# Performance work log

Measured on AMD Instinct MI355X. Metric: run time of the kernel, lower is better.

Reference implementation:

```python
import jax, jax.numpy as jnp
import numpy as np

N_NODES = 50000
LN_EPS = 1e-5


def gcn_conv(x, src, dst, norm, W, b):
    # PyG GCNConv: h = x @ W, then symmetric-normalized scatter-add, then bias.
    h = x @ W                                   # [N, out]
    msg = h[src] * norm[:, None]                # [E+N, out] gathered, scaled
    out = jax.ops.segment_sum(msg, dst, num_segments=N_NODES)
    return out + b


def layer_norm(x, gamma, beta):
    mu = jnp.mean(x, axis=-1, keepdims=True)
    var = jnp.var(x, axis=-1, keepdims=True)
    return (x - mu) * jax.lax.rsqrt(var + LN_EPS) * gamma + beta


def setup_inputs() -> dict:
    key = jax.random.key(0)
    ks = jax.random.split(key, 8)
    N, E, D = N_NODES, 1600000, 128
    x = jax.random.normal(ks[0], (N, D), dtype=jnp.float32)
    edge_index = jax.random.randint(ks[1], (2, E), 0, N, dtype=jnp.int64)
    s = 1.0 / np.sqrt(D)
    return {
        "x": x,
        "edge_index": edge_index,
        "W1": jax.random.uniform(ks[2], (D, D), jnp.float32, -s, s),
        "b1": jnp.zeros((D,), jnp.float32),
        "g1": jnp.ones((D,), jnp.float32),
        "be1": jnp.zeros((D,), jnp.float32),
        "W2": jax.random.uniform(ks[3], (D, D), jnp.float32, -s, s),
        "b2": jnp.zeros((D,), jnp.float32),
        "g2": jnp.ones((D,), jnp.float32),
        "be2": jnp.zeros((D,), jnp.float32),
    }


def reference(x, edge_index, W1, b1, g1, be1, W2, b2, g2, be2):
    # Add self-loops (PyG GCNConv default add_self_loops=True)
    sl = jnp.arange(N_NODES, dtype=edge_index.dtype)
    src = jnp.concatenate([edge_index[0], sl])
    dst = jnp.concatenate([edge_index[1], sl])
    # Symmetric normalization: deg^{-1/2}[src] * deg^{-1/2}[dst]
    deg = jax.ops.segment_sum(jnp.ones_like(src, dtype=x.dtype), dst,
                              num_segments=N_NODES)
    dinv = jnp.where(deg > 0, jax.lax.rsqrt(deg), 0.0)
    norm = dinv[src] * dinv[dst]

    h = gcn_conv(x, src, dst, norm, W1, b1)
    h = jax.nn.elu(layer_norm(h, g1, be1))
    h = gcn_conv(h, src, dst, norm, W2, b2)
    h = jax.nn.elu(layer_norm(h, g2, be2))
    return h
```

## Files before the change

kernel.cpp:

```cpp
#include <hip/hip_runtime.h>
#include <hip/hip_bf16.h>
#include <math.h>

#define N_NODES 50000
#define D 128
#define LN_EPS 1e-5f
#define NB 391
#define CHUNK 4096

typedef unsigned int u32;
typedef unsigned short u16;
typedef __attribute__((ext_vector_type(8))) short bf16x8;
typedef __attribute__((ext_vector_type(4))) float f32x4;

static __device__ __forceinline__ u16 f2bf(float f) {
    union { float f; unsigned u; } v; v.f = f;
    unsigned r = v.u + 0x7fff + ((v.u >> 16) & 1);
    return (u16)(r >> 16);
}
static __device__ __forceinline__ float bf2f(u16 b) {
    union { unsigned u; float f; } v; v.u = ((unsigned)b) << 16;
    return v.f;
}

__global__ __launch_bounds__(256) void bucket_hist(const int* __restrict__ dstA,
                                                   u32* __restrict__ bucketCount, int E) {
    __shared__ u32 hist[NB];
    for (int b = threadIdx.x; b < NB; b += 256) hist[b] = 0;
    __syncthreads();
    int stride = gridDim.x * 256;
    for (int e = blockIdx.x * 256 + threadIdx.x; e < E; e += stride)
        atomicAdd(&hist[((u32)dstA[e]) >> 7], 1u);
    __syncthreads();
    for (int b = threadIdx.x; b < NB; b += 256)
        if (hist[b]) atomicAdd(&bucketCount[b], hist[b]);
}

__global__ void scan_kernel(const u32* __restrict__ bucketCount, u32* __restrict__ ebStart,
                            u32* __restrict__ ebCursor, u32* __restrict__ csrStart) {
    __shared__ u32 s[512];
    int t = threadIdx.x;
    u32 my = (t < NB) ? bucketCount[t] : 0u;
    s[t] = my;
    __syncthreads();
    for (int off = 1; off < 512; off <<= 1) {
        u32 v = s[t] + ((t >= off) ? s[t - off] : 0u);
        __syncthreads();
        s[t] = v;
        __syncthreads();
    }
    if (t < NB) {
        u32 excl = s[t] - my;
        ebStart[t]  = excl;
        ebCursor[t] = excl;
        csrStart[t] = excl + 128u * (u32)t;
    }
}

__global__ __launch_bounds__(256) void partition_kernel(const int* __restrict__ srcA,
                                                        const int* __restrict__ dstA,
                                                        u32* __restrict__ ebCursor,
                                                        u32* __restrict__ ebuf, int E) {
    __shared__ u32 cntA[NB], cntB[NB], base[NB];
    int t = threadIdx.x;
    for (int b = t; b < NB; b += 256) { cntA[b] = 0; cntB[b] = 0; }
    __syncthreads();
    int e0 = blockIdx.x * CHUNK;
    int e1 = min(e0 + CHUNK, E);
    for (int e = e0 + t; e < e1; e += 256)
        atomicAdd(&cntA[((u32)dstA[e]) >> 7], 1u);
    __syncthreads();
    for (int b = t; b < NB; b += 256)
        if (cntA[b]) base[b] = atomicAdd(&ebCursor[b], cntA[b]);
    __syncthreads();
    for (int e = e0 + t; e < e1; e += 256) {
        u32 d = (u32)dstA[e], sv = (u32)srcA[e];
        u32 b = d >> 7;
        u32 off = atomicAdd(&cntB[b], 1u);
        ebuf[base[b] + off] = (sv << 16) | d;
    }
}

__global__ __launch_bounds__(256) void bucket_build(const u32* __restrict__ ebuf,
                                                    const u32* __restrict__ ebStart,
                                                    const u32* __restrict__ ebEnd,
                                                    const u32* __restrict__ csrStart,
                                                    u16* __restrict__ csr_src,
                                                    int* __restrict__ startArr,
                                                    int* __restrict__ deg,
                                                    float* __restrict__ dinv) {
    int b = blockIdx.x, t = threadIdx.x;
    int nodeBase = b << 7;
    int nNodes = min(128, N_NODES - nodeBase);
    __shared__ u32 cnt[128], sc[128], cur[128];
    if (t < 128) cnt[t] = 0;
    __syncthreads();
    u32 eb0 = ebStart[b], eb1 = ebEnd[b];
    for (u32 e = eb0 + t; e < eb1; e += 256)
        atomicAdd(&cnt[ebuf[e] & 127u], 1u);
    __syncthreads();
    if (t < 128) sc[t] = (t < nNodes) ? cnt[t] + 1u : 0u;
    __syncthreads();
    for (int off = 1; off < 128; off <<= 1) {
        u32 v = 0;
        if (t < 128) v = sc[t] + ((t >= off) ? sc[t - off] : 0u);
        __syncthreads();
        if (t < 128) sc[t] = v;
        __syncthreads();
    }
    u32 cs = csrStart[b];
    if (t < nNodes) {
        u32 val = cnt[t] + 1u;
        u32 excl = sc[t] - val;
        int i = nodeBase + t;
        deg[i] = (int)val;
        dinv[i] = rsqrtf((float)val);
        u32 sa = cs + excl;
        startArr[i] = (int)sa;
        csr_src[sa] = (u16)i;
        cur[t] = excl + 1u;
    }
    __syncthreads();
    for (u32 e = eb0 + t; e < eb1; e += 256) {
        u32 p = ebuf[e];
        u32 pos = atomicAdd(&cur[p & 127u], 1u);
        csr_src[cs + pos] = (u16)(p >> 16);
    }
}

static __device__ __forceinline__ bf16x8 packf8(const float* p) {
    float4 f0 = *(const float4*)p;
    float4 f1 = *(const float4*)(p + 4);
    bf16x8 r;
    r[0] = (short)f2bf(f0.x); r[1] = (short)f2bf(f0.y);
    r[2] = (short)f2bf(f0.z); r[3] = (short)f2bf(f0.w);
    r[4] = (short)f2bf(f1.x); r[5] = (short)f2bf(f1.y);
    r[6] = (short)f2bf(f1.z); r[7] = (short)f2bf(f1.w);
    return r;
}

template <int SRCF32>
__global__ __launch_bounds__(256) void gemm_mfma(const void* __restrict__ Xv,
                                                 const float* __restrict__ W,
                                                 u16* __restrict__ H, int n) {
    __shared__ __align__(16) u16 WT[D][136];
    for (int idx = threadIdx.x; idx < D * D; idx += 256) {
        int k = idx >> 7, c = idx & 127;
        WT[c][k] = f2bf(W[idx]);
    }
    __syncthreads();

    int lane = threadIdx.x & 63;
    int wid  = threadIdx.x >> 6;
    int r    = lane & 15;
    int kg   = lane >> 4;

    int rb0 = blockIdx.x * 4 + wid;
    int nrb = gridDim.x * 4;
    for (int rb = rb0; rb < n / 16; rb += nrb) {
        int row0 = rb * 16;
        bf16x8 a0, a1, a2, a3;
        if (SRCF32) {
            const float* xp = (const float*)Xv + (size_t)(row0 + r) * D + kg * 8;
            a0 = packf8(xp); a1 = packf8(xp + 32); a2 = packf8(xp + 64); a3 = packf8(xp + 96);
        } else {
            const u16* xp = (const u16*)Xv + (size_t)(row0 + r) * D + kg * 8;
            a0 = *(const bf16x8*)(xp);      a1 = *(const bf16x8*)(xp + 32);
            a2 = *(const bf16x8*)(xp + 64); a3 = *(const bf16x8*)(xp + 96);
        }
#pragma unroll
        for (int tile = 0; tile < 8; ++tile) {
            const u16* wp = &WT[tile * 16 + r][kg * 8];
            f32x4 acc = {0.f, 0.f, 0.f, 0.f};
            acc = __builtin_amdgcn_mfma_f32_16x16x32_bf16(a0, *(const bf16x8*)(wp),      acc, 0, 0, 0);
            acc = __builtin_amdgcn_mfma_f32_16x16x32_bf16(a1, *(const bf16x8*)(wp + 32), acc, 0, 0, 0);
            acc = __builtin_amdgcn_mfma_f32_16x16x32_bf16(a2, *(const bf16x8*)(wp + 64), acc, 0, 0, 0);
            acc = __builtin_amdgcn_mfma_f32_16x16x32_bf16(a3, *(const bf16x8*)(wp + 96), acc, 0, 0, 0);
#pragma unroll
            for (int i = 0; i < 4; ++i)
                H[(size_t)(row0 + kg * 4 + i) * D + tile * 16 + r] = f2bf(acc[i]);
        }
    }
}

template <int WRITE_BF16>
__global__ __launch_bounds__(256) void agg_ln_elu(
        const u16* __restrict__ H, const u16* __restrict__ csr_src,
        const int* __restrict__ startArr, const int* __restrict__ deg,
        const float* __restrict__ dinv,
        const float* __restrict__ bias, const float* __restrict__ gamma,
        const float* __restrict__ beta, void* __restrict__ outv) {
    int lane = threadIdx.x & 63;
    int wid  = threadIdx.x >> 6;
    int half = lane >> 5;
    int l    = lane & 31;
    int node = blockIdx.x * 8 + wid * 2 + half;

    int s    = startArr[node];
    int cnt  = deg[node];
    float dn = dinv[node];
    int c0   = l * 4;

    float a0 = 0.f, a1 = 0.f, a2 = 0.f, a3 = 0.f;
    int j = 0;
    for (; j + 4 <= cnt; j += 4) {
        u32 s0 = csr_src[s + j],     s1 = csr_src[s + j + 1];
        u32 s2 = csr_src[s + j + 2], s3 = csr_src[s + j + 3];
        float w0 = dinv[s0] * dn, w1 = dinv[s1] * dn;
        float w2 = dinv[s2] * dn, w3 = dinv[s3] * dn;
        ushort4 g0 = *(const ushort4*)&H[(size_t)s0 * D + c0];
        ushort4 g1 = *(const ushort4*)&H[(size_t)s1 * D + c0];
        ushort4 g2 = *(const ushort4*)&H[(size_t)s2 * D + c0];
        ushort4 g3 = *(const ushort4*)&H[(size_t)s3 * D + c0];
        a0 = fmaf(w0, bf2f(g0.x), a0); a1 = fmaf(w0, bf2f(g0.y), a1);
        a2 = fmaf(w0, bf2f(g0.z), a2); a3 = fmaf(w0, bf2f(g0.w), a3);
        a0 = fmaf(w1, bf2f(g1.x), a0); a1 = fmaf(w1, bf2f(g1.y), a1);
        a2 = fmaf(w1, bf2f(g1.z), a2); a3 = fmaf(w1, bf2f(g1.w), a3);
        a0 = fmaf(w2, bf2f(g2.x), a0); a1 = fmaf(w2, bf2f(g2.y), a1);
        a2 = fmaf(w2, bf2f(g2.z), a2); a3 = fmaf(w2, bf2f(g2.w), a3);
        a0 = fmaf(w3, bf2f(g3.x), a0); a1 = fmaf(w3, bf2f(g3.y), a1);
        a2 = fmaf(w3, bf2f(g3.z), a2); a3 = fmaf(w3, bf2f(g3.w), a3);
    }
    for (; j < cnt; ++j) {
        u32 s0 = csr_src[s + j];
        float w0 = dinv[s0] * dn;
        ushort4 g0 = *(const ushort4*)&H[(size_t)s0 * D + c0];
        a0 = fmaf(w0, bf2f(g0.x), a0); a1 = fmaf(w0, bf2f(g0.y), a1);
        a2 = fmaf(w0, bf2f(g0.z), a2); a3 = fmaf(w0, bf2f(g0.w), a3);
    }

    float4 bv = *(const float4*)&bias[c0];
    a0 += bv.x; a1 += bv.y; a2 += bv.z; a3 += bv.w;

    float sum = a0 + a1 + a2 + a3;
    float sq  = a0 * a0 + a1 * a1 + a2 * a2 + a3 * a3;
#pragma unroll
    for (int m = 16; m > 0; m >>= 1) {
        sum += __shfl_xor(sum, m, 64);
        sq  += __shfl_xor(sq,  m, 64);
    }
    float mean = sum * (1.f / 128.f);
    float var  = sq * (1.f / 128.f) - mean * mean;
    float rstd = rsqrtf(var + LN_EPS);

    float4 gv = *(const float4*)&gamma[c0];
    float4 ev = *(const float4*)&beta[c0];
    float y0 = (a0 - mean) * rstd * gv.x + ev.x;
    float y1 = (a1 - mean) * rstd * gv.y + ev.y;
    float y2 = (a2 - mean) * rstd * gv.z + ev.z;
    float y3 = (a3 - mean) * rstd * gv.w + ev.w;
    y0 = y0 > 0.f ? y0 : expm1f(y0);
    y1 = y1 > 0.f ? y1 : expm1f(y1);
    y2 = y2 > 0.f ? y2 : expm1f(y2);
    y3 = y3 > 0.f ? y3 : expm1f(y3);

    if (WRITE_BF16) {
        ushort4 o;
        o.x = f2bf(y0); o.y = f2bf(y1); o.z = f2bf(y2); o.w = f2bf(y3);
        *(ushort4*)((u16*)outv + (size_t)node * D + c0) = o;
    } else {
        float4 o; o.x = y0; o.y = y1; o.z = y2; o.w = y3;
        *(float4*)((float*)outv + (size_t)node * D + c0) = o;
    }
}

extern "C" void kernel_launch(void* const* d_in, const int* in_sizes, int n_in,
                              void* d_out, int out_size, void* d_ws, size_t ws_size,
                              hipStream_t stream) {
    const float* x   = (const float*)d_in[0];
    const int*  eidx = (const int*)d_in[1];
    const float* W1  = (const float*)d_in[2];
    const float* b1  = (const float*)d_in[3];
    const float* g1  = (const float*)d_in[4];
    const float* be1 = (const float*)d_in[5];
    const float* W2  = (const float*)d_in[6];
    const float* b2  = (const float*)d_in[7];
    const float* g2  = (const float*)d_in[8];
    const float* be2 = (const float*)d_in[9];

    int E = in_sizes[1] / 2;
    const int* srcA = eidx;
    const int* dstA = eidx + E;

    char* p = (char*)d_ws;
    auto alloc = [&](size_t bytes) {
        char* r = p;
        p += (bytes + 255) & ~(size_t)255;
        return r;
    };
    u32*   bucketCount = (u32*)alloc((size_t)NB * 4);
    u32*   ebStart     = (u32*)alloc((size_t)NB * 4);
    u32*   ebCursor    = (u32*)alloc((size_t)NB * 4);
    u32*   csrStart    = (u32*)alloc((size_t)NB * 4);
    u32*   ebuf        = (u32*)alloc((size_t)E * 4);
    u16*   csr_src     = (u16*)alloc((size_t)(E + N_NODES) * 2);
    int*   startArr    = (int*)alloc((size_t)N_NODES * 4);
    int*   deg         = (int*)alloc((size_t)N_NODES * 4);
    float* dinv        = (float*)alloc((size_t)N_NODES * 4);
    u16*   h           = (u16*)alloc((size_t)N_NODES * D * 2);
    u16*   x2b         = (u16*)alloc((size_t)N_NODES * D * 2);
    float* outp        = (float*)d_out;

    int pb = (E + CHUNK - 1) / CHUNK;
    int gb = (N_NODES / 16 + 3) / 4;
    int ab = N_NODES / 8;

    hipMemsetAsync(bucketCount, 0, (size_t)NB * 4, stream);
    bucket_hist     <<<512, 256, 0, stream>>>(dstA, bucketCount, E);
    scan_kernel     <<<1, 512, 0, stream>>>(bucketCount, ebStart, ebCursor, csrStart);
    partition_kernel<<<pb, 256, 0, stream>>>(srcA, dstA, ebCursor, ebuf, E);
    bucket_build    <<<NB, 256, 0, stream>>>(ebuf, ebStart, ebCursor, csrStart,
                                             csr_src, startArr, deg, dinv);

    gemm_mfma<1>  <<<gb, 256, 0, stream>>>(x, W1, h, N_NODES);
    agg_ln_elu<1> <<<ab, 256, 0, stream>>>(h, csr_src, startArr, deg, dinv,
                                           b1, g1, be1, x2b);
    gemm_mfma<0>  <<<gb, 256, 0, stream>>>(x2b, W2, h, N_NODES);
    agg_ln_elu<0> <<<ab, 256, 0, stream>>>(h, csr_src, startArr, deg, dinv,
                                           b2, g2, be2, outp);
}
```

Before: 295.3 us.

## Fuse GEMM1 with bucket histogram, drop scan kernel, widen aggregation unroll

The first GEMM and the destination-bucket histogram now run as one launch, with the blocks split by role. The separate scan kernel is removed: each partition block recomputes the bucket prefix scan itself, and bucket_build sums its prefix directly from the bucket counts. This cuts kernel launches and the serial single-block stage, at the cost of redundant scan work in every block. Separately, the aggregation loop is unrolled to 8 edges with two accumulator sets for more memory-level parallelism, and the final fp32 output uses nontemporal stores.

```diff
diff --git a/kernel.cpp b/kernel.cpp
--- a/kernel.cpp
+++ b/kernel.cpp
@@ -7,6 +7,8 @@
 #define LN_EPS 1e-5f
 #define NB 391
 #define CHUNK 4096
+#define GB 782
+#define HB 512
 
 typedef unsigned int u32;
 typedef unsigned short u16;
@@ -23,57 +25,130 @@
     return v.f;
 }
 
-__global__ __launch_bounds__(256) void bucket_hist(const int* __restrict__ dstA,
-                                                   u32* __restrict__ bucketCount, int E) {
+static __device__ __forceinline__ bf16x8 packf8(const float* p) {
+    float4 f0 = *(const float4*)p;
+    float4 f1 = *(const float4*)(p + 4);
+    bf16x8 r;
+    r[0] = (short)f2bf(f0.x); r[1] = (short)f2bf(f0.y);
+    r[2] = (short)f2bf(f0.z); r[3] = (short)f2bf(f0.w);
+    r[4] = (short)f2bf(f1.x); r[5] = (short)f2bf(f1.y);
+    r[6] = (short)f2bf(f1.z); r[7] = (short)f2bf(f1.w);
+    return r;
+}
+
+__global__ __launch_bounds__(256) void gemm1_hist(const float* __restrict__ X,
+                                                  const float* __restrict__ W,
+                                                  u16* __restrict__ H,
+                                                  const int* __restrict__ dstA,
+                                                  u32* __restrict__ bucketCount, int E) {
+    __shared__ __align__(16) u16 WT[D][136];
     __shared__ u32 hist[NB];
-    for (int b = threadIdx.x; b < NB; b += 256) hist[b] = 0;
-    __syncthreads();
-    int stride = gridDim.x * 256;
-    for (int e = blockIdx.x * 256 + threadIdx.x; e < E; e += stride)
-        atomicAdd(&hist[((u32)dstA[e]) >> 7], 1u);
-    __syncthreads();
-    for (int b = threadIdx.x; b < NB; b += 256)
-        if (hist[b]) atomicAdd(&bucketCount[b], hist[b]);
-}
-
-__global__ void scan_kernel(const u32* __restrict__ bucketCount, u32* __restrict__ ebStart,
-                            u32* __restrict__ ebCursor, u32* __restrict__ csrStart) {
-    __shared__ u32 s[512];
+
+    if (blockIdx.x >= GB) {
+        for (int b = threadIdx.x; b < NB; b += 256) hist[b] = 0;
+        __syncthreads();
+        int stride = HB * 256;
+        for (int e = (blockIdx.x - GB) * 256 + threadIdx.x; e < E; e += stride)
+            atomicAdd(&hist[((u32)dstA[e]) >> 7], 1u);
+        __syncthreads();
+        for (int b = threadIdx.x; b < NB; b += 256)
+            if (hist[b]) atomicAdd(&bucketCount[b], hist[b]);
+        return;
+    }
+    for (int idx = threadIdx.x; idx < D * D; idx += 256) {
+        int k = idx >> 7, c = idx & 127;
+        WT[c][k] = f2bf(W[idx]);
+    }
+    __syncthreads();
+
+    int lane = threadIdx.x & 63;
+    int wid  = threadIdx.x >> 6;
+    int r    = lane & 15;
+    int kg   = lane >> 4;
+
+    for (int rb = blockIdx.x * 4 + wid; rb < N_NODES / 16; rb += GB * 4) {
+        int row0 = rb * 16;
+        const float* xp = X + (size_t)(row0 + r) * D + kg * 8;
+        bf16x8 a0 = packf8(xp);      bf16x8 a1 = packf8(xp + 32);
+        bf16x8 a2 = packf8(xp + 64); bf16x8 a3 = packf8(xp + 96);
+#pragma unroll
+        for (int tile = 0; tile < 8; ++tile) {
+            const u16* wp = &WT[tile * 16 + r][kg * 8];
+            f32x4 acc = {0.f, 0.f, 0.f, 0.f};
+            acc = __builtin_amdgcn_mfma_f32_16x16x32_bf16(a0, *(const bf16x8*)(wp),      acc, 0, 0, 0);
+            acc = __builtin_amdgcn_mfma_f32_16x16x32_bf16(a1, *(const bf16x8*)(wp + 32), acc, 0, 0, 0);
+            acc = __builtin_amdgcn_mfma_f32_16x16x32_bf16(a2, *(const bf16x8*)(wp + 64), acc, 0, 0, 0);
+            acc = __builtin_amdgcn_mfma_f32_16x16x32_bf16(a3, *(const bf16x8*)(wp + 96), acc, 0, 0, 0);
+#pragma unroll
+            for (int i = 0; i < 4; ++i)
+                H[(size_t)(row0 + kg * 4 + i) * D + tile * 16 + r] = f2bf(acc[i]);
+        }
+    }
+}
+
+__global__ __launch_bounds__(256) void gemm_mfma(const u16* __restrict__ Xb,
+                                                 const float* __restrict__ W,
+                                                 u16* __restrict__ H) {
+    __shared__ __align__(16) u16 WT[D][136];
+    for (int idx = threadIdx.x; idx < D * D; idx += 256) {
+        int k = idx >> 7, c = idx & 127;
+        WT[c][k] = f2bf(W[idx]);
+    }
+    __syncthreads();
+    int lane = threadIdx.x & 63;
+    int wid  = threadIdx.x >> 6;
+    int r    = lane & 15;
+    int kg   = lane >> 4;
+    for (int rb = blockIdx.x * 4 + wid; rb < N_NODES / 16; rb += GB * 4) {
+        int row0 = rb * 16;
+        const u16* xp = Xb + (size_t)(row0 + r) * D + kg * 8;
+        bf16x8 a0 = *(const bf16x8*)(xp);      bf16x8 a1 = *(const bf16x8*)(xp + 32);
+        bf16x8 a2 = *(const bf16x8*)(xp + 64); bf16x8 a3 = *(const bf16x8*)(xp + 96);
+#pragma unroll
+        for (int tile = 0; tile < 8; ++tile) {
+            const u16* wp = &WT[tile * 16 + r][kg * 8];
+            f32x4 acc = {0.f, 0.f, 0.f, 0.f};
+            acc = __builtin_amdgcn_mfma_f32_16x16x32_bf16(a0, *(const bf16x8*)(wp),      acc, 0, 0, 0);
+            acc = __builtin_amdgcn_mfma_f32_16x16x32_bf16(a1, *(const bf16x8*)(wp + 32), acc, 0, 0, 0);
+            acc = __builtin_amdgcn_mfma_f32_16x16x32_bf16(a2, *(const bf16x8*)(wp + 64), acc, 0, 0, 0);
+            acc = __builtin_amdgcn_mfma_f32_16x16x32_bf16(a3, *(const bf16x8*)(wp + 96), acc, 0, 0, 0);
+#pragma unroll
+            for (int i = 0; i < 4; ++i)
+                H[(size_t)(row0 + kg * 4 + i) * D + tile * 16 + r] = f2bf(acc[i]);
+        }
+    }
+}
+
+__global__ __launch_bounds__(512) void partition_kernel(const int* __restrict__ srcA,
+                                                        const int* __restrict__ dstA,
+                                                        const u32* __restrict__ bucketCount,
+                                                        u32* __restrict__ relCursor,
+                                                        u32* __restrict__ ebuf, int E) {
+    __shared__ u32 sc[512];
+    __shared__ u32 ebS[NB], cntA[NB], cntB[NB], base[NB];
     int t = threadIdx.x;
-    u32 my = (t < NB) ? bucketCount[t] : 0u;
-    s[t] = my;
+    u32 bc = (t < NB) ? bucketCount[t] : 0u;
+    sc[t] = bc;
+    for (int b = t; b < NB; b += 512) { cntA[b] = 0; cntB[b] = 0; }
     __syncthreads();
     for (int off = 1; off < 512; off <<= 1) {
-        u32 v = s[t] + ((t >= off) ? s[t - off] : 0u);
-        __syncthreads();
-        s[t] = v;
-        __syncthreads();
-    }
-    if (t < NB) {
-        u32 excl = s[t] - my;
-        ebStart[t]  = excl;
-        ebCursor[t] = excl;
-        csrStart[t] = excl + 128u * (u32)t;
-    }
-}
-
-__global__ __launch_bounds__(256) void partition_kernel(const int* __restrict__ srcA,
-                                                        const int* __restrict__ dstA,
-                                                        u32* __restrict__ ebCursor,
-                                                        u32* __restrict__ ebuf, int E) {
-    __shared__ u32 cntA[NB], cntB[NB], base[NB];
-    int t = threadIdx.x;
-    for (int b = t; b < NB; b += 256) { cntA[b] = 0; cntB[b] = 0; }
-    __syncthreads();
+        u32 v = sc[t] + ((t >= off) ? sc[t - off] : 0u);
+        __syncthreads();
+        sc[t] = v;
+        __syncthreads();
+    }
+    if (t < NB) ebS[t] = sc[t] - bc;
+    __syncthreads();
+
     int e0 = blockIdx.x * CHUNK;
     int e1 = min(e0 + CHUNK, E);
-    for (int e = e0 + t; e < e1; e += 256)
+    for (int e = e0 + t; e < e1; e += 512)
         atomicAdd(&cntA[((u32)dstA[e]) >> 7], 1u);
     __syncthreads();
-    for (int b = t; b < NB; b += 256)
-        if (cntA[b]) base[b] = atomicAdd(&ebCursor[b], cntA[b]);
-    __syncthreads();
-    for (int e = e0 + t; e < e1; e += 256) {
+    for (int b = t; b < NB; b += 512)
+        if (cntA[b]) base[b] = ebS[b] + atomicAdd(&relCursor[b], cntA[b]);
+    __syncthreads();
+    for (int e = e0 + t; e < e1; e += 512) {
         u32 d = (u32)dstA[e], sv = (u32)srcA[e];
         u32 b = d >> 7;
         u32 off = atomicAdd(&cntB[b], 1u);
@@ -82,20 +157,29 @@
 }
 
 __global__ __launch_bounds__(256) void bucket_build(const u32* __restrict__ ebuf,
-                                                    const u32* __restrict__ ebStart,
-                                                    const u32* __restrict__ ebEnd,
-                                                    const u32* __restrict__ csrStart,
+                                                    const u32* __restrict__ bucketCount,
                                                     u16* __restrict__ csr_src,
                                                     int* __restrict__ startArr,
                                                     int* __restrict__ deg,
                                                     float* __restrict__ dinv) {
     int b = blockIdx.x, t = threadIdx.x;
+    __shared__ u32 red[256];
+    __shared__ u32 cnt[128], sc[128], cur[128];
+    u32 partial = 0;
+    for (int i = t; i < b; i += 256) partial += bucketCount[i];
+    red[t] = partial;
+    if (t < 128) cnt[t] = 0;
+    __syncthreads();
+    for (int off = 128; off > 0; off >>= 1) {
+        if (t < off) red[t] += red[t + off];
+        __syncthreads();
+    }
+    u32 eb0 = red[0];
+    u32 eb1 = eb0 + bucketCount[b];
+    u32 cs  = eb0 + 128u * (u32)b;
+
     int nodeBase = b << 7;
     int nNodes = min(128, N_NODES - nodeBase);
-    __shared__ u32 cnt[128], sc[128], cur[128];
-    if (t < 128) cnt[t] = 0;
-    __syncthreads();
-    u32 eb0 = ebStart[b], eb1 = ebEnd[b];
     for (u32 e = eb0 + t; e < eb1; e += 256)
         atomicAdd(&cnt[ebuf[e] & 127u], 1u);
     __syncthreads();
@@ -108,7 +192,6 @@
         if (t < 128) sc[t] = v;
         __syncthreads();
     }
-    u32 cs = csrStart[b];
     if (t < nNodes) {
         u32 val = cnt[t] + 1u;
         u32 excl = sc[t] - val;
@@ -125,61 +208,6 @@
         u32 p = ebuf[e];
         u32 pos = atomicAdd(&cur[p & 127u], 1u);
         csr_src[cs + pos] = (u16)(p >> 16);
-    }
-}
-
-static __device__ __forceinline__ bf16x8 packf8(const float* p) {
-    float4 f0 = *(const float4*)p;
-    float4 f1 = *(const float4*)(p + 4);
-    bf16x8 r;
-    r[0] = (short)f2bf(f0.x); r[1] = (short)f2bf(f0.y);
-    r[2] = (short)f2bf(f0.z); r[3] = (short)f2bf(f0.w);
-    r[4] = (short)f2bf(f1.x); r[5] = (short)f2bf(f1.y);
-    r[6] = (short)f2bf(f1.z); r[7] = (short)f2bf(f1.w);
-    return r;
-}
-
-template <int SRCF32>
-__global__ __launch_bounds__(256) void gemm_mfma(const void* __restrict__ Xv,
-                                                 const float* __restrict__ W,
-                                                 u16* __restrict__ H, int n) {
-    __shared__ __align__(16) u16 WT[D][136];
-    for (int idx = threadIdx.x; idx < D * D; idx += 256) {
-        int k = idx >> 7, c = idx & 127;
-        WT[c][k] = f2bf(W[idx]);
-    }
-    __syncthreads();
-
-    int lane = threadIdx.x & 63;
-    int wid  = threadIdx.x >> 6;
-    int r    = lane & 15;
-    int kg   = lane >> 4;
-
-    int rb0 = blockIdx.x * 4 + wid;
-    int nrb = gridDim.x * 4;
-    for (int rb = rb0; rb < n / 16; rb += nrb) {
-        int row0 = rb * 16;
-        bf16x8 a0, a1, a2, a3;
-        if (SRCF32) {
-            const float* xp = (const float*)Xv + (size_t)(row0 + r) * D + kg * 8;
-            a0 = packf8(xp); a1 = packf8(xp + 32); a2 = packf8(xp + 64); a3 = packf8(xp + 96);
-        } else {
-            const u16* xp = (const u16*)Xv + (size_t)(row0 + r) * D + kg * 8;
-            a0 = *(const bf16x8*)(xp);      a1 = *(const bf16x8*)(xp + 32);
-            a2 = *(const bf16x8*)(xp + 64); a3 = *(const bf16x8*)(xp + 96);
-        }
-#pragma unroll
-        for (int tile = 0; tile < 8; ++tile) {
-            const u16* wp = &WT[tile * 16 + r][kg * 8];
-            f32x4 acc = {0.f, 0.f, 0.f, 0.f};
-            acc = __builtin_amdgcn_mfma_f32_16x16x32_bf16(a0, *(const bf16x8*)(wp),      acc, 0, 0, 0);
-            acc = __builtin_amdgcn_mfma_f32_16x16x32_bf16(a1, *(const bf16x8*)(wp + 32), acc, 0, 0, 0);
-            acc = __builtin_amdgcn_mfma_f32_16x16x32_bf16(a2, *(const bf16x8*)(wp + 64), acc, 0, 0, 0);
-            acc = __builtin_amdgcn_mfma_f32_16x16x32_bf16(a3, *(const bf16x8*)(wp + 96), acc, 0, 0, 0);
-#pragma unroll
-            for (int i = 0; i < 4; ++i)
-                H[(size_t)(row0 + kg * 4 + i) * D + tile * 16 + r] = f2bf(acc[i]);
-        }
     }
 }
 
@@ -202,32 +230,50 @@
     int c0   = l * 4;
 
     float a0 = 0.f, a1 = 0.f, a2 = 0.f, a3 = 0.f;
+    float b0 = 0.f, b1 = 0.f, b2 = 0.f, b3 = 0.f;
     int j = 0;
-    for (; j + 4 <= cnt; j += 4) {
-        u32 s0 = csr_src[s + j],     s1 = csr_src[s + j + 1];
-        u32 s2 = csr_src[s + j + 2], s3 = csr_src[s + j + 3];
-        float w0 = dinv[s0] * dn, w1 = dinv[s1] * dn;
-        float w2 = dinv[s2] * dn, w3 = dinv[s3] * dn;
-        ushort4 g0 = *(const ushort4*)&H[(size_t)s0 * D + c0];
-        ushort4 g1 = *(const ushort4*)&H[(size_t)s1 * D + c0];
-        ushort4 g2 = *(const ushort4*)&H[(size_t)s2 * D + c0];
-        ushort4 g3 = *(const ushort4*)&H[(size_t)s3 * D + c0];
+    for (; j + 8 <= cnt; j += 8) {
+        u32 i0 = csr_src[s + j],     i1 = csr_src[s + j + 1];
+        u32 i2 = csr_src[s + j + 2], i3 = csr_src[s + j + 3];
+        u32 i4 = csr_src[s + j + 4], i5 = csr_src[s + j + 5];
+        u32 i6 = csr_src[s + j + 6], i7 = csr_src[s + j + 7];
+        float w0 = dinv[i0] * dn, w1 = dinv[i1] * dn;
+        float w2 = dinv[i2] * dn, w3 = dinv[i3] * dn;
+        float w4 = dinv[i4] * dn, w5 = dinv[i5] * dn;
+        float w6 = dinv[i6] * dn, w7 = dinv[i7] * dn;
+        ushort4 g0 = *(const ushort4*)&H[(size_t)i0 * D + c0];
+        ushort4 g1 = *(const ushort4*)&H[(size_t)i1 * D + c0];
+        ushort4 g2 = *(const ushort4*)&H[(size_t)i2 * D + c0];
+        ushort4 g3 = *(const ushort4*)&H[(size_t)i3 * D + c0];
+        ushort4 g4 = *(const ushort4*)&H[(size_t)i4 * D + c0];
+        ushort4 g5 = *(const ushort4*)&H[(size_t)i5 * D + c0];
+        ushort4 g6 = *(const ushort4*)&H[(size_t)i6 * D + c0];
+        ushort4 g7 = *(const ushort4*)&H[(size_t)i7 * D + c0];
         a0 = fmaf(w0, bf2f(g0.x), a0); a1 = fmaf(w0, bf2f(g0.y), a1);
         a2 = fmaf(w0, bf2f(g0.z), a2); a3 = fmaf(w0, bf2f(g0.w), a3);
-        a0 = fmaf(w1, bf2f(g1.x), a0); a1 = fmaf(w1, bf2f(g1.y), a1);
-        a2 = fmaf(w1, bf2f(g1.z), a2); a3 = fmaf(w1, bf2f(g1.w), a3);
+        b0 = fmaf(w1, bf2f(g1.x), b0); b1 = fmaf(w1, bf2f(g1.y), b1);
+        b2 = fmaf(w1, bf2f(g1.z), b2); b3 = fmaf(w1, bf2f(g1.w), b3);
         a0 = fmaf(w2, bf2f(g2.x), a0); a1 = fmaf(w2, bf2f(g2.y), a1);
         a2 = fmaf(w2, bf2f(g2.z), a2); a3 = fmaf(w2, bf2f(g2.w), a3);
-        a0 = fmaf(w3, bf2f(g3.x), a0); a1 = fmaf(w3, bf2f(g3.y), a1);
-        a2 = fmaf(w3, bf2f(g3.z), a2); a3 = fmaf(w3, bf2f(g3.w), a3);
+        b0 = fmaf(w3, bf2f(g3.x), b0); b1 = fmaf(w3, bf2f(g3.y), b1);
+        b2 = fmaf(w3, bf2f(g3.z), b2); b3 = fmaf(w3, bf2f(g3.w), b3);
+        a0 = fmaf(w4, bf2f(g4.x), a0); a1 = fmaf(w4, bf2f(g4.y), a1);
+        a2 = fmaf(w4, bf2f(g4.z), a2); a3 = fmaf(w4, bf2f(g4.w), a3);
+        b0 = fmaf(w5, bf2f(g5.x), b0); b1 = fmaf(w5, bf2f(g5.y), b1);
+        b2 = fmaf(w5, bf2f(g5.z), b2); b3 = fmaf(w5, bf2f(g5.w), b3);
+        a0 = fmaf(w6, bf2f(g6.x), a0); a1 = fmaf(w6, bf2f(g6.y), a1);
+        a2 = fmaf(w6, bf2f(g6.z), a2); a3 = fmaf(w6, bf2f(g6.w), a3);
+        b0 = fmaf(w7, bf2f(g7.x), b0); b1 = fmaf(w7, bf2f(g7.y), b1);
+        b2 = fmaf(w7, bf2f(g7.z), b2); b3 = fmaf(w7, bf2f(g7.w), b3);
     }
     for (; j < cnt; ++j) {
-        u32 s0 = csr_src[s + j];
-        float w0 = dinv[s0] * dn;
-        ushort4 g0 = *(const ushort4*)&H[(size_t)s0 * D + c0];
+        u32 i0 = csr_src[s + j];
+        float w0 = dinv[i0] * dn;
+        ushort4 g0 = *(const ushort4*)&H[(size_t)i0 * D + c0];
         a0 = fmaf(w0, bf2f(g0.x), a0); a1 = fmaf(w0, bf2f(g0.y), a1);
         a2 = fmaf(w0, bf2f(g0.z), a2); a3 = fmaf(w0, bf2f(g0.w), a3);
     }
+    a0 += b0; a1 += b1; a2 += b2; a3 += b3;
 
     float4 bv = *(const float4*)&bias[c0];
     a0 += bv.x; a1 += bv.y; a2 += bv.z; a3 += bv.w;
@@ -259,8 +305,8 @@
         o.x = f2bf(y0); o.y = f2bf(y1); o.z = f2bf(y2); o.w = f2bf(y3);
         *(ushort4*)((u16*)outv + (size_t)node * D + c0) = o;
     } else {
-        float4 o; o.x = y0; o.y = y1; o.z = y2; o.w = y3;
-        *(float4*)((float*)outv + (size_t)node * D + c0) = o;
+        f32x4 o = {y0, y1, y2, y3};
+        __builtin_nontemporal_store(o, (f32x4*)((float*)outv + (size_t)node * D + c0));
     }
 }
 
@@ -288,34 +334,29 @@
         p += (bytes + 255) & ~(size_t)255;
         return r;
     };
-    u32*   bucketCount = (u32*)alloc((size_t)NB * 4);
-    u32*   ebStart     = (u32*)alloc((size_t)NB * 4);
-    u32*   ebCursor    = (u32*)alloc((size_t)NB * 4);
-    u32*   csrStart    = (u32*)alloc((size_t)NB * 4);
-    u32*   ebuf        = (u32*)alloc((size_t)E * 4);
-    u16*   csr_src     = (u16*)alloc((size_t)(E + N_NODES) * 2);
-    int*   startArr    = (int*)alloc((size_t)N_NODES * 4);
-    int*   deg         = (int*)alloc((size_t)N_NODES * 4);
-    float* dinv        = (float*)alloc((size_t)N_NODES * 4);
-    u16*   h           = (u16*)alloc((size_t)N_NODES * D * 2);
-    u16*   x2b         = (u16*)alloc((size_t)N_NODES * D * 2);
-    float* outp        = (float*)d_out;
+    u32*   ctr      = (u32*)alloc((size_t)1024 * 4);
+    u32*   ebuf     = (u32*)alloc((size_t)E * 4);
+    u16*   csr_src  = (u16*)alloc((size_t)(E + N_NODES) * 2);
+    int*   startArr = (int*)alloc((size_t)N_NODES * 4);
+    int*   deg      = (int*)alloc((size_t)N_NODES * 4);
+    float* dinv     = (float*)alloc((size_t)N_NODES * 4);
+    u16*   h        = (u16*)alloc((size_t)N_NODES * D * 2);
+    u16*   x2b      = (u16*)alloc((size_t)N_NODES * D * 2);
+    float* outp     = (float*)d_out;
+
+    u32* bucketCount = ctr;
+    u32* relCursor   = ctr + 512;
 
     int pb = (E + CHUNK - 1) / CHUNK;
-    int gb = (N_NODES / 16 + 3) / 4;
     int ab = N_NODES / 8;
 
-    hipMemsetAsync(bucketCount, 0, (size_t)NB * 4, stream);
-    bucket_hist     <<<512, 256, 0, stream>>>(dstA, bucketCount, E);
-    scan_kernel     <<<1, 512, 0, stream>>>(bucketCount, ebStart, ebCursor, csrStart);
-    partition_kernel<<<pb, 256, 0, stream>>>(srcA, dstA, ebCursor, ebuf, E);
-    bucket_build    <<<NB, 256, 0, stream>>>(ebuf, ebStart, ebCursor, csrStart,
-                                             csr_src, startArr, deg, dinv);
-
-    gemm_mfma<1>  <<<gb, 256, 0, stream>>>(x, W1, h, N_NODES);
-    agg_ln_elu<1> <<<ab, 256, 0, stream>>>(h, csr_src, startArr, deg, dinv,
-                                           b1, g1, be1, x2b);
-    gemm_mfma<0>  <<<gb, 256, 0, stream>>>(x2b, W2, h, N_NODES);
-    agg_ln_elu<0> <<<ab, 256, 0, stream>>>(h, csr_src, startArr, deg, dinv,
-                                           b2, g2, be2, outp);
-}
+    hipMemsetAsync(ctr, 0, 1024 * 4, stream);
+    gemm1_hist      <<<GB + HB, 256, 0, stream>>>(x, W1, h, dstA, bucketCount, E);
+    partition_kernel<<<pb, 512, 0, stream>>>(srcA, dstA, bucketCount, relCursor, ebuf, E);
+    bucket_build    <<<NB, 256, 0, stream>>>(ebuf, bucketCount, csr_src, startArr, deg, dinv);
+    agg_ln_elu<1>   <<<ab, 256, 0, stream>>>(h, csr_src, startArr, deg, dinv,
+                                             b1, g1, be1, x2b);
+    gemm_mfma       <<<GB, 256, 0, stream>>>(x2b, W2, h);
+    agg_ln_elu<0>   <<<ab, 256, 0, stream>>>(h, csr_src, startArr, deg, dinv,
+                                             b2, g2, be2, outp);
+}
```

Result: faster. 285.6 us (-3.3%).
